# Optimization experiments

Hardware: AMD Instinct MI355X
Metric: run time of the kernel (lower is better)

The kernel has to match this reference:

```python
import jax, jax.numpy as jnp
import numpy as np
import math

KMAX = 4
K_FLOOR = 1e-6
NUM_GRAPHS = 32

def _k_lattice():
    r = np.arange(-KMAX, KMAX + 1)
    I, J, Kk = np.meshgrid(r, r, r, indexing='ij')
    lat = np.stack([I, J, Kk], axis=-1).reshape(-1, 3).astype(np.float32)
    lat = lat[np.any(lat != 0, axis=1)]  # exclude k=0 (include_k0=False)
    return jnp.asarray(lat)  # [K,3], K=728

def setup_inputs() -> dict:
    key = jax.random.key(0)
    ks = jax.random.split(key, 10)
    N, B, C, H = 8192, NUM_GRAPHS, 4, 64
    pos = jax.random.uniform(ks[0], (N, 3), dtype=jnp.float32) * 10.0
    batch = jnp.sort(jax.random.randint(ks[1], (N,), 0, B)).astype(jnp.int32)
    cell = jnp.eye(3, dtype=jnp.float32)[None] * 12.0 + 0.2 * jax.random.normal(ks[2], (B, 3, 3), dtype=jnp.float32)
    source = 0.1 * jax.random.normal(ks[3], (N, C), dtype=jnp.float32)
    W1 = jax.random.normal(ks[4], (3, H), dtype=jnp.float32) * (1.0 / math.sqrt(3))
    b1 = jnp.zeros((H,), jnp.float32)
    W2 = jax.random.normal(ks[5], (H, H), dtype=jnp.float32) * (1.0 / math.sqrt(H))
    b2 = jnp.zeros((H,), jnp.float32)
    W3 = jax.random.normal(ks[6], (H, 1), dtype=jnp.float32) * (1.0 / math.sqrt(H))
    b3 = jnp.zeros((1,), jnp.float32)
    return {"pos": pos, "batch": batch, "cell": cell, "source": source,
            "W1": W1, "b1": b1, "W2": W2, "b2": b2, "W3": W3, "b3": b3}

def reference(pos, batch, cell, source, W1, b1, W2, b2, W3, b3):
    two_pi = 2.0 * math.pi
    klat = _k_lattice()                              # [K,3]
    B = cell.shape[0]
    inv_cells = jnp.linalg.inv(cell)                 # [B,3,3]
    # fractional coords and phases
    frac = jnp.einsum('ni,nij->nj', pos, inv_cells[batch])   # [N,3]
    phases = two_pi * (frac @ klat.T)                # [N,K]
    cosP = jnp.cos(phases)
    sinP = jnp.sin(phases)
    # structure factors via segment-sum over graphs
    w_cos = source[:, None, :] * cosP[:, :, None]    # [N,K,C]
    w_sin = source[:, None, :] * sinP[:, :, None]
    S_cos = jax.ops.segment_sum(w_cos, batch, num_segments=B)  # [B,K,C]
    S_sin = jax.ops.segment_sum(w_sin, batch, num_segments=B)
    # k-space radial filter
    k_cart = two_pi * jnp.einsum('kd,bdh->bkh', klat, inv_cells)  # [B,K,3]
    k_norms = jnp.linalg.norm(k_cart, axis=-1)       # [B,K]
    safe_k = jnp.maximum(k_norms, K_FLOOR)
    x0 = jnp.log1p(safe_k)
    feat = jnp.stack([x0, x0 * x0, 1.0 / safe_k], axis=-1)       # [B,K,3]
    h = jax.nn.silu(feat @ W1 + b1)
    h = jax.nn.silu(h @ W2 + b2)
    scale = jax.nn.softplus((h @ W3 + b3)[..., 0])   # [B,K]
    w = (4.0 * math.pi / (safe_k * safe_k)) * scale
    w = jnp.where(k_norms > K_FLOOR, w, 0.0)         # include_k0=False
    volumes = jnp.maximum(jnp.abs(jnp.linalg.det(cell)), K_FLOOR)  # [B]
    # per-atom potential
    t_cos = w[batch] * cosP                          # [N,K]
    t_sin = w[batch] * sinP
    potential = (jnp.einsum('nk,nkc->nc', t_cos, S_cos[batch]) +
                 jnp.einsum('nk,nkc->nc', t_sin, S_sin[batch])) / volumes[batch][:, None]
    atom_energy = 0.5 * jnp.sum(source * potential, axis=-1, keepdims=True)  # [N,1]
    return atom_energy
```

## Files before the change

### kernel.cpp

```cpp
#include <hip/hip_runtime.h>
#include <math.h>

#define N_ATOMS 8192
#define NGRAPH  32
#define KHALF   364
#define TWO_PI  6.28318530717958647692f
#define CH      384


__device__ __forceinline__ float silu_f(float x) {
    return x / (1.0f + __expf(-x));
}

__device__ __forceinline__ void screv(float rev, float* s, float* c) {
    float f = rev - floorf(rev);
    *s = __builtin_amdgcn_sinf(f);
    *c = __builtin_amdgcn_cosf(f);
}

__device__ __forceinline__ void inv3x3(const float* __restrict__ c, float* iv, float* detOut) {
    float a00 = c[0], a01 = c[1], a02 = c[2];
    float a10 = c[3], a11 = c[4], a12 = c[5];
    float a20 = c[6], a21 = c[7], a22 = c[8];
    float c00 = a11 * a22 - a12 * a21;
    float c01 = a12 * a20 - a10 * a22;
    float c02 = a10 * a21 - a11 * a20;
    float det = a00 * c00 + a01 * c01 + a02 * c02;
    float r = 1.0f / det;
    iv[0] = c00 * r; iv[1] = (a02 * a21 - a01 * a22) * r; iv[2] = (a01 * a12 - a02 * a11) * r;
    iv[3] = c01 * r; iv[4] = (a00 * a22 - a02 * a20) * r; iv[5] = (a02 * a10 - a00 * a12) * r;
    iv[6] = c02 * r; iv[7] = (a01 * a20 - a00 * a21) * r; iv[8] = (a00 * a11 - a01 * a10) * r;
    *detOut = det;
}

__device__ __forceinline__ int lower_bound_wave(const int* __restrict__ batch, int v, int lane) {
    int x = batch[lane * 128];
    int c1 = __popcll(__ballot(x < v));
    int lo2 = (c1 > 0 ? c1 - 1 : 0) * 128;
    int y = batch[lo2 + lane * 2];
    int c2 = __popcll(__ballot(y < v));
    if (c2 == 0) return lo2;
    int cand = lo2 + 2 * c2;
    return (batch[cand - 1] < v) ? cand : cand - 1;
}

__device__ __forceinline__ void stage_atom(
    float2 (* __restrict__ atab)[17], float4* __restrict__ srcs, int a,
    float px, float py, float pz, float4 msrc, const float* __restrict__ iv,
    int g, int jA0, int jA1, int jB0, int jB1)
{
    float r1 = px * iv[0] + py * iv[3] + pz * iv[6];
    float r2 = px * iv[1] + py * iv[4] + pz * iv[7];
    float r3 = px * iv[2] + py * iv[5] + pz * iv[8];
    float s1, c1; screv(r1, &s1, &c1);
    float s2, c2; screv(r2, &s2, &c2);
    float s3, c3; screv(r3, &s3, &c3);
    float c1_2 = c1 * c1 - s1 * s1, s1_2 = 2.f * c1 * s1;
    float cg_, sg_;
    if (g == 1)      { cg_ = c1;   sg_ = s1; }
    else if (g == 2) { cg_ = c1_2; sg_ = s1_2; }
    else if (g == 3) { cg_ = c1_2 * c1 - s1_2 * s1; sg_ = s1_2 * c1 + c1_2 * s1; }
    else             { cg_ = c1_2 * c1_2 - s1_2 * s1_2; sg_ = 2.f * c1_2 * s1_2; }
    atab[a][0] = make_float2(cg_, -sg_);
    float c2_2 = c2 * c2 - s2 * s2, s2_2 = 2.f * c2 * s2;
    float c2_4 = c2_2 * c2_2 - s2_2 * s2_2, s2_4 = 2.f * c2_2 * s2_2;
    float ec, es;
    if (jA0 == 0) { ec = c2_4; es = -s2_4; } else { ec = c2; es = s2; }
    int slot = 1;
    for (int m = jA0; m < jA1; ++m) {
        atab[a][slot] = make_float2(ec, es); ++slot;
        float t = ec * c2 - es * s2; es = ec * s2 + es * c2; ec = t;
    }
    if (jB1 > jB0) {
        int q = 4 - jB0;
        float qc, qs;
        if (q == 4)      { qc = c2_4; qs = s2_4; }
        else if (q == 3) { qc = c2_2 * c2 - s2_2 * s2; qs = s2_2 * c2 + c2_2 * s2; }
        else if (q == 2) { qc = c2_2; qs = s2_2; }
        else             { qc = c2;   qs = s2; }
        ec = qc; es = -qs;
        for (int m = jB0; m < jB1; ++m) {
            atab[a][slot] = make_float2(ec, es); ++slot;
            float t = ec * c2 - es * s2; es = ec * s2 + es * c2; ec = t;
        }
    }
    float c3_2 = c3 * c3 - s3 * s3, s3_2 = 2.f * c3 * s3;
    float c3_4 = c3_2 * c3_2 - s3_2 * s3_2, s3_4 = 2.f * c3_2 * s3_2;
    ec = c3_4; es = -s3_4;
    #pragma unroll
    for (int m = 0; m < 9; ++m) {
        atab[a][7 + m] = make_float2(ec, es);
        float t = ec * c3 - es * s3; es = ec * s3 + es * c3; ec = t;
    }
    srcs[a] = msrc;
}

__global__ __launch_bounds__(512, 1) void kAll(
    const float* __restrict__ cell, const float* __restrict__ pos,
    const int* __restrict__ batch, const float* __restrict__ source,
    const float* __restrict__ W1, const float* __restrict__ b1,
    const float* __restrict__ W2, const float* __restrict__ b2,
    const float* __restrict__ W3, const float* __restrict__ b3,
    float* __restrict__ out)
{
    __shared__ float  lwts[4484];
    __shared__ float2 atab[CH][17];
    __shared__ float4 srcs[CH];
    __shared__ float4 partC[7][64];
    __shared__ float4 partS[7][64];
    __shared__ float  comb[512];
    __shared__ float  lw[64];
    __shared__ float4 lSc[64];
    __shared__ float4 lSs[64];
    __shared__ int    sbounds[2];

    int bid = blockIdx.x;
    int tid = threadIdx.x;
    int gb = bid >> 3;
    int b  = bid & 7;

    int pA, jA0, jA1, jB0, jB1, nsegA, nel;
    if (b < 4) { pA = b;     jA0 = 0; jA1 = 5; jB0 = 0; jB1 = 0; nsegA = 45; nel = 45; }
    else       { pA = b - 4; jA0 = 5; jA1 = 9;
                 jB0 = b - 4; jB1 = (b == 7) ? 5 : (b - 3);
                 nsegA = 36; nel = 36 + (jB1 - jB0) * 9; }
    int nrA   = jA1 - jA0;
    int nrows = nrA + (jB1 - jB0);
    int g = 4 - pA;

    int kl = tid & 63;
    int h  = tid >> 6;

    if (h < 6) {
        for (int i = tid; i < 1120; i += 384) {
            float4 v; int o;
            if (i < 48)        { v = ((const float4*)W1)[i];      o = i * 4; }
            else if (i < 64)   { v = ((const float4*)b1)[i - 48]; o = 192 + (i - 48) * 4; }
            else if (i < 1088) { v = ((const float4*)W2)[i - 64]; o = 256 + (i - 64) * 4; }
            else if (i < 1104) { v = ((const float4*)b2)[i - 1088]; o = 4352 + (i - 1088) * 4; }
            else               { v = ((const float4*)W3)[i - 1104]; o = 4416 + (i - 1104) * 4; }
            *((float4*)&lwts[o]) = v;
        }
        if (tid == 0) lwts[4480] = b3[0];
    } else {
        int lb = lower_bound_wave(batch, gb + (h - 6), kl);
        if (kl == 0) sbounds[h - 6] = lb;
    }

    float iv[9]; float det;
    inv3x3(cell + gb * 9, iv, &det);
    float vol = fmaxf(fabsf(det), 1e-6f);

    int el = kl;
    int pe, jje, lle;
    if (el < nsegA) { pe = pA; jje = jA0 + el / 9; lle = el % 9; }
    else            { int e2 = el - nsegA; pe = 4; jje = jB0 + e2 / 9; lle = e2 % 9; }
    int rrl = el / 9;
    int hk = pe * 81 + jje * 9 + lle;
    bool evalid = (el < nel) && (hk < KHALF);

    __syncthreads();

    int s0 = sbounds[0], e0 = sbounds[1];
    int len = e0 - s0;
    int cnt0 = min(CH, len);
    bool multi = len > CH;

    float px0 = 0.f, py0 = 0.f, pz0 = 0.f;
    float4 msrc = make_float4(0.f, 0.f, 0.f, 0.f);
    if (tid < cnt0) {
        int n = s0 + tid;
        px0 = pos[n * 3]; py0 = pos[n * 3 + 1]; pz0 = pos[n * 3 + 2];
        msrc = ((const float4*)source)[n];
    }

    float kn, sk;
    {
        float fi = (float)(pe - 4);
        float fj = (float)(jje - 4);
        float fl = (float)(lle - 4);
        float kx = TWO_PI * (fi * iv[0] + fj * iv[3] + fl * iv[6]);
        float ky = TWO_PI * (fi * iv[1] + fj * iv[4] + fl * iv[7]);
        float kz = TWO_PI * (fi * iv[2] + fj * iv[5] + fl * iv[8]);
        kn = sqrtf(kx * kx + ky * ky + kz * kz);
        sk = fmaxf(kn, 1e-6f);
        float x0 = log1pf(sk);
        float f0 = x0, f1 = x0 * x0, f2 = 1.0f / sk;

        float acc[8];
        #pragma unroll
        for (int j = 0; j < 8; ++j) acc[j] = lwts[4352 + h * 8 + j];
        for (int i = 0; i < 64; ++i) {
            float a_ = lwts[192 + i] + f0 * lwts[i] + f1 * lwts[64 + i] + f2 * lwts[128 + i];
            float hh = silu_f(a_);
            const float* w2row = &lwts[256 + i * 64 + h * 8];
            #pragma unroll
            for (int j = 0; j < 8; ++j) acc[j] = fmaf(hh, w2row[j], acc[j]);
        }
        float partial = 0.f;
        #pragma unroll
        for (int j = 0; j < 8; ++j) partial += silu_f(acc[j]) * lwts[4416 + h * 8 + j];
        comb[tid] = partial;
    }

    if (tid < cnt0)
        stage_atom(atab, srcs, tid, px0, py0, pz0, msrc, iv, g, jA0, jA1, jB0, jB1);
    __syncthreads();

    float4 accC = make_float4(0.f, 0.f, 0.f, 0.f);
    float4 accS = make_float4(0.f, 0.f, 0.f, 0.f);
    if (evalid) {
        for (int a = h; a < cnt0; a += 8) {
            float2 tj = atab[a][1 + rrl];
            float2 tl = atab[a][7 + lle];
            float tic, tis;
            if (el < nsegA) {
                float2 fI = atab[a][0];
                tic = fI.x * tj.x - fI.y * tj.y;
                tis = fI.x * tj.y + fI.y * tj.x;
            } else { tic = tj.x; tis = tj.y; }
            float cv = tic * tl.x - tis * tl.y;
            float sv = tic * tl.y + tis * tl.x;
            float4 s = srcs[a];
            accC.x = fmaf(s.x, cv, accC.x); accC.y = fmaf(s.y, cv, accC.y);
            accC.z = fmaf(s.z, cv, accC.z); accC.w = fmaf(s.w, cv, accC.w);
            accS.x = fmaf(s.x, sv, accS.x); accS.y = fmaf(s.y, sv, accS.y);
            accS.z = fmaf(s.z, sv, accS.z); accS.w = fmaf(s.w, sv, accS.w);
        }
    }

    for (int base = s0 + CH; base < e0; base += CH) {
        int cnt = min(CH, e0 - base);
        __syncthreads();
        if (tid < cnt) {
            int n = base + tid;
            float px = pos[n * 3], py = pos[n * 3 + 1], pz = pos[n * 3 + 2];
            float4 ms = ((const float4*)source)[n];
            stage_atom(atab, srcs, tid, px, py, pz, ms, iv, g, jA0, jA1, jB0, jB1);
        }
        __syncthreads();
        if (evalid) {
            for (int a = h; a < cnt; a += 8) {
                float2 tj = atab[a][1 + rrl];
                float2 tl = atab[a][7 + lle];
                float tic, tis;
                if (el < nsegA) {
                    float2 fI = atab[a][0];
                    tic = fI.x * tj.x - fI.y * tj.y;
                    tis = fI.x * tj.y + fI.y * tj.x;
                } else { tic = tj.x; tis = tj.y; }
                float cv = tic * tl.x - tis * tl.y;
                float sv = tic * tl.y + tis * tl.x;
                float4 s = srcs[a];
                accC.x = fmaf(s.x, cv, accC.x); accC.y = fmaf(s.y, cv, accC.y);
                accC.z = fmaf(s.z, cv, accC.z); accC.w = fmaf(s.w, cv, accC.w);
                accS.x = fmaf(s.x, sv, accS.x); accS.y = fmaf(s.y, sv, accS.y);
                accS.z = fmaf(s.z, sv, accS.z); accS.w = fmaf(s.w, sv, accS.w);
            }
        }
    }

    if (h > 0) {
        partC[h - 1][kl] = accC;
        partS[h - 1][kl] = accS;
    }
    __syncthreads();
    if (h == 0) {
        #pragma unroll
        for (int qq = 0; qq < 7; ++qq) {
            float4 pc = partC[qq][kl], ps = partS[qq][kl];
            accC.x += pc.x; accC.y += pc.y; accC.z += pc.z; accC.w += pc.w;
            accS.x += ps.x; accS.y += ps.y; accS.z += ps.z; accS.w += ps.w;
        }
        lSc[kl] = accC;
        lSs[kl] = accS;
    } else if (h == 1) {
        float mlp = lwts[4480];
        #pragma unroll
        for (int w = 0; w < 8; ++w) mlp += comb[kl + 64 * w];
        float sc = (mlp > 20.0f) ? mlp : log1pf(__expf(mlp));
        float wgt = (12.566370614359172954f / (sk * sk)) * sc;
        if (!(kn > 1e-6f)) wgt = 0.0f;
        lw[kl] = evalid ? (wgt / vol) : 0.0f;
    }
    __syncthreads();

    int half = tid >> 8;
    int rsplit = (nrows + 1) >> 1;
    int r0 = half ? rsplit : 0;
    int r1 = half ? nrows  : rsplit;

    if (!multi) {
        for (int na = (tid & 255); na < len; na += 256) {
            float2 fI = atab[na][0];
            float4 s  = srcs[na];
            float acc = 0.f;
            for (int rr = r0; rr < r1; ++rr) {
                float2 tj = atab[na][1 + rr];
                float rjc, rjs;
                if (rr < nrA) {
                    rjc = fI.x * tj.x - fI.y * tj.y;
                    rjs = fI.x * tj.y + fI.y * tj.x;
                } else {
                    rjc = tj.x; rjs = tj.y;
                }
                #pragma unroll
                for (int ll = 0; ll < 9; ++ll) {
                    float2 tl = atab[na][7 + ll];
                    float fc = rjc * tl.x - rjs * tl.y;
                    float fs = rjc * tl.y + rjs * tl.x;
                    int e = rr * 9 + ll;
                    float4 C  = lSc[e];
                    float4 S4 = lSs[e];
                    float w_  = lw[e];
                    float dc = s.x * C.x  + s.y * C.y  + s.z * C.z  + s.w * C.w;
                    float ds = s.x * S4.x + s.y * S4.y + s.z * S4.z + s.w * S4.w;
                    acc = fmaf(w_, fmaf(fc, dc, fs * ds), acc);
                }
            }
            atomicAdd(&out[s0 + na], acc);
        }
    } else {
        for (int na = (tid & 255); na < len; na += 256) {
            int n = s0 + na;
            float px = pos[n * 3], py = pos[n * 3 + 1], pz = pos[n * 3 + 2];
            float r1v = px * iv[0] + py * iv[3] + pz * iv[6];
            float r2v = px * iv[1] + py * iv[4] + pz * iv[7];
            float r3v = px * iv[2] + py * iv[5] + pz * iv[8];
            float s1, c1; screv(r1v, &s1, &c1);
            float s2, c2; screv(r2v, &s2, &c2);
            float s3, c3; screv(r3v, &s3, &c3);
            float c3_2 = c3 * c3 - s3 * s3, s3_2 = 2.f * c3 * s3;
            float c3_4 = c3_2 * c3_2 - s3_2 * s3_2, s3_4 = 2.f * c3_2 * s3_2;
            float c2_2 = c2 * c2 - s2 * s2, s2_2 = 2.f * c2 * s2;
            float c2_4 = c2_2 * c2_2 - s2_2 * s2_2, s2_4 = 2.f * c2_2 * s2_2;
            float4 s = ((const float4*)source)[n];
            float acc = 0.f;
            int rr = 0;
            {
                float c1_2 = c1 * c1 - s1 * s1, s1_2 = 2.f * c1 * s1;
                float cg_, sg_;
                if (g == 1)      { cg_ = c1;   sg_ = s1; }
                else if (g == 2) { cg_ = c1_2; sg_ = s1_2; }
                else if (g == 3) { cg_ = c1_2 * c1 - s1_2 * s1; sg_ = s1_2 * c1 + c1_2 * s1; }
                else             { cg_ = c1_2 * c1_2 - s1_2 * s1_2; sg_ = 2.f * c1_2 * s1_2; }
                float ci0 = cg_, si0 = -sg_;
                float ejc, ejs;
                if (jA0 == 0) { ejc = ci0 * c2_4 + si0 * s2_4; ejs = si0 * c2_4 - ci0 * s2_4; }
                else          { ejc = ci0 * c2 - si0 * s2;     ejs = si0 * c2 + ci0 * s2; }
                for (int jj = jA0; jj < jA1; ++jj, ++rr) {
                    if (rr >= r0 && rr < r1) {
                        float fc = ejc * c3_4 + ejs * s3_4;
                        float fs = ejs * c3_4 - ejc * s3_4;
                        #pragma unroll
                        for (int ll = 0; ll < 9; ++ll) {
                            int e = rr * 9 + ll;
                            float4 C  = lSc[e];
                            float4 S4 = lSs[e];
                            float w_  = lw[e];
                            float dc = s.x * C.x  + s.y * C.y  + s.z * C.z  + s.w * C.w;
                            float ds = s.x * S4.x + s.y * S4.y + s.z * S4.z + s.w * S4.w;
                            acc = fmaf(w_, fmaf(fc, dc, fs * ds), acc);
                            float nfc = fc * c3 - fs * s3;
                            fs = fc * s3 + fs * c3;
                            fc = nfc;
                        }
                    }
                    float t = ejc * c2 - ejs * s2; ejs = ejc * s2 + ejs * c2; ejc = t;
                }
            }
            if (jB1 > jB0) {
                float ejc = c2_4, ejs = -s2_4;
                for (int t2 = 0; t2 < jB0; ++t2) {
                    float t = ejc * c2 - ejs * s2; ejs = ejc * s2 + ejs * c2; ejc = t;
                }
                for (int jj = jB0; jj < jB1; ++jj, ++rr) {
                    if (rr >= r0 && rr < r1) {
                        float fc = ejc * c3_4 + ejs * s3_4;
                        float fs = ejs * c3_4 - ejc * s3_4;
                        #pragma unroll
                        for (int ll = 0; ll < 9; ++ll) {
                            int e = rr * 9 + ll;
                            float4 C  = lSc[e];
                            float4 S4 = lSs[e];
                            float w_  = lw[e];
                            float dc = s.x * C.x  + s.y * C.y  + s.z * C.z  + s.w * C.w;
                            float ds = s.x * S4.x + s.y * S4.y + s.z * S4.z + s.w * S4.w;
                            acc = fmaf(w_, fmaf(fc, dc, fs * ds), acc);
                            float nfc = fc * c3 - fs * s3;
                            fs = fc * s3 + fs * c3;
                            fc = nfc;
                        }
                    }
                    float t = ejc * c2 - ejs * s2; ejs = ejc * s2 + ejs * c2; ejc = t;
                }
            }
            atomicAdd(&out[n], acc);
        }
    }
}

extern "C" void kernel_launch(void* const* d_in, const int* in_sizes, int n_in,
                              void* d_out, int out_size, void* d_ws, size_t ws_size,
                              hipStream_t stream)
{
    const float* pos    = (const float*)d_in[0];
    const int*   batch  = (const int*)d_in[1];
    const float* cell   = (const float*)d_in[2];
    const float* source = (const float*)d_in[3];
    const float* W1 = (const float*)d_in[4];
    const float* b1 = (const float*)d_in[5];
    const float* W2 = (const float*)d_in[6];
    const float* b2 = (const float*)d_in[7];
    const float* W3 = (const float*)d_in[8];
    const float* b3 = (const float*)d_in[9];
    float* out = (float*)d_out;
    (void)d_ws; (void)ws_size;

    kAll<<<dim3(NGRAPH * 8), 512, 0, stream>>>(cell, pos, batch, source,
        W1, b1, W2, b2, W3, b3, out);
}
```

Measured before the change: 91.46 us.

## Premultiply i-phase into row table, share MLP layer-1 via LDS, reorder block mapping

Folds the per-atom i-direction phase into the stored j-row phase factors at staging time, removing a complex multiply from the inner structure-factor and potential loops. The first MLP layer is computed once per hidden unit into a new shared array instead of being recomputed redundantly by each of the eight thread groups. Block-to-graph mapping is changed so consecutive blocks cover different graphs, and a prefetch of pos/source is issued with an empty asm to keep it alive, likely to warm caches. This adds 16KB of LDS and an extra barrier.

```diff
diff --git a/kernel.cpp b/kernel.cpp
--- a/kernel.cpp
+++ b/kernel.cpp
@@ -61,11 +61,13 @@
     else if (g == 2) { cg_ = c1_2; sg_ = s1_2; }
     else if (g == 3) { cg_ = c1_2 * c1 - s1_2 * s1; sg_ = s1_2 * c1 + c1_2 * s1; }
     else             { cg_ = c1_2 * c1_2 - s1_2 * s1_2; sg_ = 2.f * c1_2 * s1_2; }
-    atab[a][0] = make_float2(cg_, -sg_);
+    float fic = cg_, fis = -sg_;
     float c2_2 = c2 * c2 - s2 * s2, s2_2 = 2.f * c2 * s2;
     float c2_4 = c2_2 * c2_2 - s2_2 * s2_2, s2_4 = 2.f * c2_2 * s2_2;
-    float ec, es;
-    if (jA0 == 0) { ec = c2_4; es = -s2_4; } else { ec = c2; es = s2; }
+    float bc, bs;
+    if (jA0 == 0) { bc = c2_4; bs = -s2_4; } else { bc = c2; bs = s2; }
+    float ec = fic * bc - fis * bs;
+    float es = fic * bs + fis * bc;
     int slot = 1;
     for (int m = jA0; m < jA1; ++m) {
         atab[a][slot] = make_float2(ec, es); ++slot;
@@ -104,6 +106,7 @@
     float* __restrict__ out)
 {
     __shared__ float  lwts[4484];
+    __shared__ float  h1s[4096];
     __shared__ float2 atab[CH][17];
     __shared__ float4 srcs[CH];
     __shared__ float4 partC[7][64];
@@ -116,22 +119,30 @@
 
     int bid = blockIdx.x;
     int tid = threadIdx.x;
-    int gb = bid >> 3;
-    int b  = bid & 7;
+    int gb = bid & 31;
+    int b  = bid >> 5;
 
     int pA, jA0, jA1, jB0, jB1, nsegA, nel;
     if (b < 4) { pA = b;     jA0 = 0; jA1 = 5; jB0 = 0; jB1 = 0; nsegA = 45; nel = 45; }
     else       { pA = b - 4; jA0 = 5; jA1 = 9;
                  jB0 = b - 4; jB1 = (b == 7) ? 5 : (b - 3);
                  nsegA = 36; nel = 36 + (jB1 - jB0) * 9; }
-    int nrA   = jA1 - jA0;
-    int nrows = nrA + (jB1 - jB0);
+    int nrows = (jA1 - jA0) + (jB1 - jB0);
     int g = 4 - pA;
 
     int kl = tid & 63;
     int h  = tid >> 6;
 
+    float wa = 0.f, wb = 0.f, wc = 0.f, wd = 0.f;
     if (h < 6) {
+        int n0 = gb * 256 - 16; if (n0 < 0) n0 = 0;
+        if (tid < 192) {
+            float4 v = ((const float4*)pos)[(n0 * 3) / 4 + tid];
+            wa = v.x; wb = v.y; wc = v.z; wd = v.w;
+        } else {
+            float4 v = ((const float4*)source)[n0 + tid - 192];
+            wa = v.x; wb = v.y; wc = v.z; wd = v.w;
+        }
         for (int i = tid; i < 1120; i += 384) {
             float4 v; int o;
             if (i < 48)        { v = ((const float4*)W1)[i];      o = i * 4; }
@@ -142,6 +153,7 @@
             *((float4*)&lwts[o]) = v;
         }
         if (tid == 0) lwts[4480] = b3[0];
+        asm volatile("" :: "v"(wa), "v"(wb), "v"(wc), "v"(wd));
     } else {
         int lb = lower_bound_wave(batch, gb + (h - 6), kl);
         if (kl == 0) sbounds[h - 6] = lb;
@@ -174,7 +186,7 @@
         msrc = ((const float4*)source)[n];
     }
 
-    float kn, sk;
+    float kn, sk, f0, f1, f2;
     {
         float fi = (float)(pe - 4);
         float fj = (float)(jje - 4);
@@ -185,14 +197,26 @@
         kn = sqrtf(kx * kx + ky * ky + kz * kz);
         sk = fmaxf(kn, 1e-6f);
         float x0 = log1pf(sk);
-        float f0 = x0, f1 = x0 * x0, f2 = 1.0f / sk;
-
+        f0 = x0; f1 = x0 * x0; f2 = 1.0f / sk;
+    }
+
+    {
+        int i0 = h * 8;
+        #pragma unroll
+        for (int ii = 0; ii < 8; ++ii) {
+            int i = i0 + ii;
+            float a_ = lwts[192 + i] + f0 * lwts[i] + f1 * lwts[64 + i] + f2 * lwts[128 + i];
+            h1s[i * 64 + kl] = silu_f(a_);
+        }
+    }
+    __syncthreads();
+
+    {
         float acc[8];
         #pragma unroll
         for (int j = 0; j < 8; ++j) acc[j] = lwts[4352 + h * 8 + j];
         for (int i = 0; i < 64; ++i) {
-            float a_ = lwts[192 + i] + f0 * lwts[i] + f1 * lwts[64 + i] + f2 * lwts[128 + i];
-            float hh = silu_f(a_);
+            float hh = h1s[i * 64 + kl];
             const float* w2row = &lwts[256 + i * 64 + h * 8];
             #pragma unroll
             for (int j = 0; j < 8; ++j) acc[j] = fmaf(hh, w2row[j], acc[j]);
@@ -211,16 +235,10 @@
     float4 accS = make_float4(0.f, 0.f, 0.f, 0.f);
     if (evalid) {
         for (int a = h; a < cnt0; a += 8) {
-            float2 tj = atab[a][1 + rrl];
+            float2 rj = atab[a][1 + rrl];
             float2 tl = atab[a][7 + lle];
-            float tic, tis;
-            if (el < nsegA) {
-                float2 fI = atab[a][0];
-                tic = fI.x * tj.x - fI.y * tj.y;
-                tis = fI.x * tj.y + fI.y * tj.x;
-            } else { tic = tj.x; tis = tj.y; }
-            float cv = tic * tl.x - tis * tl.y;
-            float sv = tic * tl.y + tis * tl.x;
+            float cv = rj.x * tl.x - rj.y * tl.y;
+            float sv = rj.x * tl.y + rj.y * tl.x;
             float4 s = srcs[a];
             accC.x = fmaf(s.x, cv, accC.x); accC.y = fmaf(s.y, cv, accC.y);
             accC.z = fmaf(s.z, cv, accC.z); accC.w = fmaf(s.w, cv, accC.w);
@@ -241,16 +259,10 @@
         __syncthreads();
         if (evalid) {
             for (int a = h; a < cnt; a += 8) {
-                float2 tj = atab[a][1 + rrl];
+                float2 rj = atab[a][1 + rrl];
                 float2 tl = atab[a][7 + lle];
-                float tic, tis;
-                if (el < nsegA) {
-                    float2 fI = atab[a][0];
-                    tic = fI.x * tj.x - fI.y * tj.y;
-                    tis = fI.x * tj.y + fI.y * tj.x;
-                } else { tic = tj.x; tis = tj.y; }
-                float cv = tic * tl.x - tis * tl.y;
-                float sv = tic * tl.y + tis * tl.x;
+                float cv = rj.x * tl.x - rj.y * tl.y;
+                float sv = rj.x * tl.y + rj.y * tl.x;
                 float4 s = srcs[a];
                 accC.x = fmaf(s.x, cv, accC.x); accC.y = fmaf(s.y, cv, accC.y);
                 accC.z = fmaf(s.z, cv, accC.z); accC.w = fmaf(s.w, cv, accC.w);
@@ -292,23 +304,15 @@
 
     if (!multi) {
         for (int na = (tid & 255); na < len; na += 256) {
-            float2 fI = atab[na][0];
-            float4 s  = srcs[na];
+            float4 s = srcs[na];
             float acc = 0.f;
             for (int rr = r0; rr < r1; ++rr) {
-                float2 tj = atab[na][1 + rr];
-                float rjc, rjs;
-                if (rr < nrA) {
-                    rjc = fI.x * tj.x - fI.y * tj.y;
-                    rjs = fI.x * tj.y + fI.y * tj.x;
-                } else {
-                    rjc = tj.x; rjs = tj.y;
-                }
+                float2 rj = atab[na][1 + rr];
                 #pragma unroll
                 for (int ll = 0; ll < 9; ++ll) {
                     float2 tl = atab[na][7 + ll];
-                    float fc = rjc * tl.x - rjs * tl.y;
-                    float fs = rjc * tl.y + rjs * tl.x;
+                    float fc = rj.x * tl.x - rj.y * tl.y;
+                    float fs = rj.x * tl.y + rj.y * tl.x;
                     int e = rr * 9 + ll;
                     float4 C  = lSc[e];
                     float4 S4 = lSs[e];
```

Result: faster. 85.54 us (-6.5%).
